# Kernel tuning notes

Hardware: AMD Instinct MI355X
Metric: run time of the kernel (lower is better)

The kernel has to match this reference:

```python
import jax, jax.numpy as jnp
import numpy as np

G = 4096          # number of graphs in the batch
N = 1048576       # total nodes across batch
E = 16777216      # total edges across batch
NUM_RELS = 50     # relation vocabulary


def setup_inputs() -> dict:
    key = jax.random.key(0)
    k0, k1, k2, k3, k4 = jax.random.split(key, 5)
    node_type = jax.random.randint(k0, (N,), 0, 3, dtype=jnp.int32)
    edge_type = jax.random.randint(k1, (E,), 0, NUM_RELS, dtype=jnp.int32)
    edge_index = jax.random.randint(k2, (2, E), 0, N, dtype=jnp.int32)
    edge_batch = jnp.sort(jax.random.randint(k3, (E,), 0, G, dtype=jnp.int32))
    scorer_weight = jax.random.normal(k4, (NUM_RELS * 9, 1), dtype=jnp.float32)
    return {
        "node_type": node_type,
        "edge_type": edge_type,
        "edge_index": edge_index,
        "edge_batch": edge_batch,
        "scorer_weight": scorer_weight,
        "num_graphs": G,
    }


def reference(node_type, edge_type, edge_index, edge_batch, scorer_weight, num_graphs):
    # edge encoding: et*9 + nt[src]*3 + nt[dst]   (per-edge index into table)
    enc = edge_type * 9 + node_type[edge_index[0]] * 3 + node_type[edge_index[1]]
    # embedding lookup (hidden_size == 1) -> [E]
    vals = scorer_weight[enc, 0]
    # per-graph sum of edge scores -> [G]
    per_graph = jax.ops.segment_sum(vals, edge_batch, num_segments=num_graphs)
    # torch.stack([[score], ...]) -> [G, 1]
    return per_graph[:, None]
```

## Files before the change

### kernel.cpp

```cpp
#include <hip/hip_runtime.h>

typedef int v4i __attribute__((ext_vector_type(4)));
typedef unsigned int u32;
typedef __attribute__((address_space(1))) const u32 gas_u32;
typedef __attribute__((address_space(3))) u32 las_u32;

#define THREADS 1024
#define NWAVES (THREADS / 64)
#define EPT 8
#define CHUNK (THREADS * EPT)
#define NBLK 256
#define PART_BITS 19
#define PART_NODES (1 << PART_BITS)
#define PART_WORDS (PART_NODES / 16)
#define TBL 450
#define WAVE_WORDS (PART_WORDS / NWAVES)
#define DMA_PER_WAVE (WAVE_WORDS / 256)

#define BAR() do {                                            \
    asm volatile("s_waitcnt lgkmcnt(0)" ::: "memory");        \
    __builtin_amdgcn_s_barrier();                             \
    __builtin_amdgcn_sched_barrier(0);                        \
} while (0)

#define WAITVM(n) do {                                        \
    asm volatile("s_waitcnt vmcnt(" #n ")" ::: "memory");     \
    __builtin_amdgcn_sched_barrier(0);                        \
} while (0)

__global__ void zero_kernel(float* __restrict__ out, int n) {
    int i = blockIdx.x * blockDim.x + threadIdx.x;
    if (i < n) out[i] = 0.0f;
}

__global__ void pack_nt_kernel(const int* __restrict__ nt,
                               unsigned int* __restrict__ packed,
                               int nwords, int N) {
    int i = blockIdx.x * blockDim.x + threadIdx.x;
    if (i >= nwords) return;
    unsigned int word = 0;
    int base = i * 16;
    if (base + 16 <= N) {
        #pragma unroll
        for (int j = 0; j < 4; ++j) {
            int4 v = *reinterpret_cast<const int4*>(nt + base + j * 4);
            word |= (unsigned)(v.x & 3) << (2 * (j * 4 + 0));
            word |= (unsigned)(v.y & 3) << (2 * (j * 4 + 1));
            word |= (unsigned)(v.z & 3) << (2 * (j * 4 + 2));
            word |= (unsigned)(v.w & 3) << (2 * (j * 4 + 3));
        }
    } else {
        for (int j = 0; base + j < N; ++j)
            word |= (unsigned)(nt[base + j] & 3) << (2 * j);
    }
    packed[i] = word;
}

__device__ __forceinline__ void dma_fill(const u32* __restrict__ pnt,
                                         u32* lds_base, int p, int wv, int lane) {
    const u32* g = pnt + (size_t)p * PART_WORDS + wv * WAVE_WORDS + lane * 4;
    u32* l = lds_base + wv * WAVE_WORDS;
    #pragma unroll
    for (int i = 0; i < DMA_PER_WAVE; ++i)
        __builtin_amdgcn_global_load_lds((gas_u32*)(g + i * 256),
                                         (las_u32*)(l + i * 256), 16, 0, 0);
}

__launch_bounds__(THREADS)
__global__ void edge_score_k(const u32* __restrict__ pnt,
                             const int* __restrict__ et_g,
                             const int* __restrict__ es_g,
                             const int* __restrict__ ed_g,
                             const int* __restrict__ eb_g,
                             const float* __restrict__ wt,
                             float* __restrict__ out,
                             int nchunk) {
    __shared__ __align__(16) u32 buf[PART_WORDS];
    __shared__ float lw[TBL];

    const int tid  = threadIdx.x;
    const int lane = tid & 63;
    const int wv   = tid >> 6;

    if (tid < TBL) lw[tid] = wt[tid];

    const long blk0 = (long)blockIdx.x * ((long)nchunk * CHUNK);
    const long lb   = (long)wv * (64 * EPT) + (long)lane * 4;

    v4i etv[2], svv[2], dvv[2];
    #pragma unroll
    for (int j = 0; j < 2; ++j) {
        etv[j] = __builtin_nontemporal_load((const v4i*)(et_g + blk0 + lb + j * 256));
        svv[j] = __builtin_nontemporal_load((const v4i*)(es_g + blk0 + lb + j * 256));
        dvv[j] = __builtin_nontemporal_load((const v4i*)(ed_g + blk0 + lb + j * 256));
    }

    for (int c = 0; c < nchunk; ++c) {
        const long cb = blk0 + (long)c * CHUNK + lb;

        BAR();
        dma_fill(pnt, buf, 0, wv, lane);
        v4i ebv0 = __builtin_nontemporal_load((const v4i*)(eb_g + cb));
        v4i ebv1 = __builtin_nontemporal_load((const v4i*)(eb_g + cb + 256));
        int sv[EPT], dv[EPT], enc[EPT];
        #pragma unroll
        for (int j = 0; j < 2; ++j)
            #pragma unroll
            for (int q = 0; q < 4; ++q) {
                enc[j * 4 + q] = etv[j][q] * 9;
                sv[j * 4 + q]  = svv[j][q];
                dv[j * 4 + q]  = dvv[j][q];
            }
        WAITVM(2);
        BAR();
        #pragma unroll
        for (int k = 0; k < EPT; ++k) {
            unsigned s = (unsigned)sv[k], d = (unsigned)dv[k];
            bool as = (s >> PART_BITS) == 0u;
            bool ad = (d >> PART_BITS) == 0u;
            u32 ws = buf[as ? ((s >> 4) & (PART_WORDS - 1u)) : 0u];
            u32 wd = buf[ad ? ((d >> 4) & (PART_WORDS - 1u)) : 0u];
            if (as) enc[k] += (int)((ws >> ((s & 15u) << 1)) & 3u) * 3;
            if (ad) enc[k] += (int)((wd >> ((d & 15u) << 1)) & 3u);
        }

        BAR();
        dma_fill(pnt, buf, 1, wv, lane);
        {
            long nb = (c + 1 < nchunk) ? (cb + CHUNK) : cb;
            #pragma unroll
            for (int j = 0; j < 2; ++j) {
                etv[j] = __builtin_nontemporal_load((const v4i*)(et_g + nb + j * 256));
                svv[j] = __builtin_nontemporal_load((const v4i*)(es_g + nb + j * 256));
                dvv[j] = __builtin_nontemporal_load((const v4i*)(ed_g + nb + j * 256));
            }
        }
        WAITVM(6);
        BAR();
        #pragma unroll
        for (int k = 0; k < EPT; ++k) {
            unsigned s = (unsigned)sv[k], d = (unsigned)dv[k];
            bool as = (s >> PART_BITS) == 1u;
            bool ad = (d >> PART_BITS) == 1u;
            u32 ws = buf[as ? ((s >> 4) & (PART_WORDS - 1u)) : 0u];
            u32 wd = buf[ad ? ((d >> 4) & (PART_WORDS - 1u)) : 0u];
            if (as) enc[k] += (int)((ws >> ((s & 15u) << 1)) & 3u) * 3;
            if (ad) enc[k] += (int)((wd >> ((d & 15u) << 1)) & 3u);
        }

        float val[EPT];
        #pragma unroll
        for (int k = 0; k < EPT; ++k) val[k] = lw[enc[k]];

        int wb0 = __shfl(ebv0[0], 0);
        int wbL = __shfl(ebv1[3], 63);
        if (wb0 == wbL) {
            float ssum = 0.0f;
            #pragma unroll
            for (int k = 0; k < EPT; ++k) ssum += val[k];
            #pragma unroll
            for (int off = 32; off >= 1; off >>= 1)
                ssum += __shfl_down(ssum, off);
            if (lane == 0) atomicAdd(&out[wb0], ssum);
        } else {
            float acc = 0.0f; int cur = -1;
            #pragma unroll
            for (int k = 0; k < EPT; ++k) {
                int bb = (k < 4) ? ebv0[k] : ebv1[k - 4];
                if (bb != cur) {
                    if (cur >= 0) atomicAdd(&out[cur], acc);
                    cur = bb; acc = 0.0f;
                }
                acc += val[k];
            }
            if (cur >= 0) atomicAdd(&out[cur], acc);
        }
    }
}

__global__ void edge_score_simple(const int* __restrict__ nt,
                                  const int* __restrict__ et,
                                  const int* __restrict__ es,
                                  const int* __restrict__ ed,
                                  const int* __restrict__ eb,
                                  const float* __restrict__ w,
                                  float* __restrict__ out,
                                  long e0, long E) {
    long e = e0 + (long)blockIdx.x * blockDim.x + threadIdx.x;
    if (e >= E) return;
    int enc = et[e] * 9 + nt[es[e]] * 3 + nt[ed[e]];
    atomicAdd(&out[eb[e]], w[enc]);
}

extern "C" void kernel_launch(void* const* d_in, const int* in_sizes, int n_in,
                              void* d_out, int out_size, void* d_ws, size_t ws_size,
                              hipStream_t stream) {
    const int*   node_type  = (const int*)d_in[0];
    const int*   edge_type  = (const int*)d_in[1];
    const int*   edge_index = (const int*)d_in[2];
    const int*   edge_batch = (const int*)d_in[3];
    const float* w          = (const float*)d_in[4];
    float* out = (float*)d_out;

    long N = in_sizes[0];
    long E = in_sizes[1];
    const int* esrc = edge_index;
    const int* edst = edge_index + E;

    zero_kernel<<<(out_size + 255) / 256, 256, 0, stream>>>(out, out_size);

    int  nwords = (int)((N + 15) / 16);
    long nchunk = E / ((long)NBLK * CHUNK);
    bool fast_ok = (ws_size >= (size_t)nwords * 4) &&
                   (N <= 2L * PART_NODES) && (nchunk > 0);

    if (fast_ok) {
        unsigned int* pnt = (unsigned int*)d_ws;
        pack_nt_kernel<<<(nwords + 255) / 256, 256, 0, stream>>>(node_type, pnt, nwords, (int)N);

        edge_score_k<<<NBLK, THREADS, 0, stream>>>(
            pnt, edge_type, esrc, edst, edge_batch, w, out, (int)nchunk);

        long covered = (long)NBLK * nchunk * CHUNK;
        long rem     = E - covered;
        if (rem > 0) {
            int tb = (int)((rem + 255) / 256);
            edge_score_simple<<<tb, 256, 0, stream>>>(
                node_type, edge_type, esrc, edst, edge_batch, w, out, covered, E);
        }
    } else {
        int tb = (int)((E + 255) / 256);
        edge_score_simple<<<tb, 256, 0, stream>>>(
            node_type, edge_type, esrc, edst, edge_batch, w, out, 0, E);
    }
}
```

Measured before the change: 113.8 us.

## Split node-type table into four LDS partitions with double-buffered DMA fills

Cuts the packed node-type table into four 16K-word partitions and double-buffers them in LDS, so the next partition's DMA fill overlaps the current gather phase instead of refilling a single buffer serially. Per-edge partition byte addresses and shifts are computed once and reused across the four phases, and edges outside the current partition read a zero pad word rather than branching. The edge-data prefetch of the next chunk is dropped in favour of loading at the start of each chunk. The block now goes through four barrier-separated phases per chunk, and each edge does eight LDS reads instead of four, which adds sync and LDS traffic.

After: 152.5 us. 34.1% more time.

```diff
diff --git a/kernel.cpp b/kernel.cpp
--- a/kernel.cpp
+++ b/kernel.cpp
@@ -6,16 +6,18 @@
 typedef __attribute__((address_space(3))) u32 las_u32;
 
 #define THREADS 1024
-#define NWAVES (THREADS / 64)
+#define NWAVES 16
 #define EPT 8
 #define CHUNK (THREADS * EPT)
 #define NBLK 256
-#define PART_BITS 19
+#define PART_BITS 18
 #define PART_NODES (1 << PART_BITS)
 #define PART_WORDS (PART_NODES / 16)
+#define NPART 4
 #define TBL 450
-#define WAVE_WORDS (PART_WORDS / NWAVES)
-#define DMA_PER_WAVE (WAVE_WORDS / 256)
+#define FILL_WAVE_WORDS (PART_WORDS / NWAVES)
+#define FILL_PER_WAVE (FILL_WAVE_WORDS / 256)
+#define ZPAD_BYTE (2u * PART_WORDS * 4u)
 
 #define BAR() do {                                            \
     asm volatile("s_waitcnt lgkmcnt(0)" ::: "memory");        \
@@ -57,13 +59,33 @@
 }
 
 __device__ __forceinline__ void dma_fill(const u32* __restrict__ pnt,
-                                         u32* lds_base, int p, int wv, int lane) {
-    const u32* g = pnt + (size_t)p * PART_WORDS + wv * WAVE_WORDS + lane * 4;
-    u32* l = lds_base + wv * WAVE_WORDS;
+                                         u32* lds0, int p, int wv, int lane) {
+    const u32* g = pnt + (size_t)p * PART_WORDS + wv * FILL_WAVE_WORDS + lane * 4;
+    u32* l = lds0 + (p & 1) * PART_WORDS + wv * FILL_WAVE_WORDS;
     #pragma unroll
-    for (int i = 0; i < DMA_PER_WAVE; ++i)
+    for (int i = 0; i < FILL_PER_WAVE; ++i)
         __builtin_amdgcn_global_load_lds((gas_u32*)(g + i * 256),
                                          (las_u32*)(l + i * 256), 16, 0, 0);
+}
+
+template <int P>
+__device__ __forceinline__ void gather_phase(const u32* lds0,
+                                             const u32 (&axs)[EPT], const u32 (&axd)[EPT],
+                                             const u32 (&shs)[EPT], const u32 (&shd)[EPT],
+                                             int (&enc)[EPT]) {
+    #pragma unroll
+    for (int k = 0; k < EPT; ++k) {
+        u32 as = axs[k];
+        u32 aaddr = ((as & 3u) == (u32)P) ? (as - (u32)P) : ZPAD_BYTE;
+        u32 rs = *reinterpret_cast<const u32*>(
+                     reinterpret_cast<const char*>(lds0) + aaddr);
+        u32 ad = axd[k];
+        u32 daddr = ((ad & 3u) == (u32)P) ? (ad - (u32)P) : ZPAD_BYTE;
+        u32 rd = *reinterpret_cast<const u32*>(
+                     reinterpret_cast<const char*>(lds0) + daddr);
+        enc[k] += (int)((rs >> shs[k]) & 3u) * 3;
+        enc[k] += (int)((rd >> shd[k]) & 3u);
+    }
 }
 
 __launch_bounds__(THREADS)
@@ -75,85 +97,80 @@
                              const float* __restrict__ wt,
                              float* __restrict__ out,
                              int nchunk) {
-    __shared__ __align__(16) u32 buf[PART_WORDS];
-    __shared__ float lw[TBL];
+    __shared__ __align__(16) u32 lds_all[2 * PART_WORDS + 16 + TBL];
+    u32* lds0 = lds_all;
+    float* lw = reinterpret_cast<float*>(lds_all + 2 * PART_WORDS + 16);
 
     const int tid  = threadIdx.x;
     const int lane = tid & 63;
     const int wv   = tid >> 6;
 
-    if (tid < TBL) lw[tid] = wt[tid];
+    if (tid < 16) lds_all[2 * PART_WORDS + tid] = 0u;
+    for (int i = tid; i < TBL; i += THREADS) lw[i] = wt[i];
+
+    dma_fill(pnt, lds0, 0, wv, lane);
 
     const long blk0 = (long)blockIdx.x * ((long)nchunk * CHUNK);
     const long lb   = (long)wv * (64 * EPT) + (long)lane * 4;
 
-    v4i etv[2], svv[2], dvv[2];
-    #pragma unroll
-    for (int j = 0; j < 2; ++j) {
-        etv[j] = __builtin_nontemporal_load((const v4i*)(et_g + blk0 + lb + j * 256));
-        svv[j] = __builtin_nontemporal_load((const v4i*)(es_g + blk0 + lb + j * 256));
-        dvv[j] = __builtin_nontemporal_load((const v4i*)(ed_g + blk0 + lb + j * 256));
-    }
-
     for (int c = 0; c < nchunk; ++c) {
         const long cb = blk0 + (long)c * CHUNK + lb;
 
         BAR();
-        dma_fill(pnt, buf, 0, wv, lane);
-        v4i ebv0 = __builtin_nontemporal_load((const v4i*)(eb_g + cb));
-        v4i ebv1 = __builtin_nontemporal_load((const v4i*)(eb_g + cb + 256));
-        int sv[EPT], dv[EPT], enc[EPT];
+        v4i et0 = __builtin_nontemporal_load((const v4i*)(et_g + cb));
+        v4i et1 = __builtin_nontemporal_load((const v4i*)(et_g + cb + 256));
+        v4i sv0 = __builtin_nontemporal_load((const v4i*)(es_g + cb));
+        v4i sv1 = __builtin_nontemporal_load((const v4i*)(es_g + cb + 256));
+        v4i dv0 = __builtin_nontemporal_load((const v4i*)(ed_g + cb));
+        v4i dv1 = __builtin_nontemporal_load((const v4i*)(ed_g + cb + 256));
+        __builtin_amdgcn_sched_barrier(0);
+        dma_fill(pnt, lds0, 1, wv, lane);
+
+        int enc[EPT]; u32 axs[EPT], axd[EPT], shs[EPT], shd[EPT];
         #pragma unroll
-        for (int j = 0; j < 2; ++j)
-            #pragma unroll
-            for (int q = 0; q < 4; ++q) {
-                enc[j * 4 + q] = etv[j][q] * 9;
-                sv[j * 4 + q]  = svv[j][q];
-                dv[j * 4 + q]  = dvv[j][q];
-            }
-        WAITVM(2);
-        BAR();
-        #pragma unroll
-        for (int k = 0; k < EPT; ++k) {
-            unsigned s = (unsigned)sv[k], d = (unsigned)dv[k];
-            bool as = (s >> PART_BITS) == 0u;
-            bool ad = (d >> PART_BITS) == 0u;
-            u32 ws = buf[as ? ((s >> 4) & (PART_WORDS - 1u)) : 0u];
-            u32 wd = buf[ad ? ((d >> 4) & (PART_WORDS - 1u)) : 0u];
-            if (as) enc[k] += (int)((ws >> ((s & 15u) << 1)) & 3u) * 3;
-            if (ad) enc[k] += (int)((wd >> ((d & 15u) << 1)) & 3u);
-        }
-
-        BAR();
-        dma_fill(pnt, buf, 1, wv, lane);
-        {
-            long nb = (c + 1 < nchunk) ? (cb + CHUNK) : cb;
-            #pragma unroll
-            for (int j = 0; j < 2; ++j) {
-                etv[j] = __builtin_nontemporal_load((const v4i*)(et_g + nb + j * 256));
-                svv[j] = __builtin_nontemporal_load((const v4i*)(es_g + nb + j * 256));
-                dvv[j] = __builtin_nontemporal_load((const v4i*)(ed_g + nb + j * 256));
-            }
-        }
+        for (int q = 0; q < 4; ++q) {
+            enc[q]     = et0[q] * 9;
+            enc[4 + q] = et1[q] * 9;
+            u32 s0 = (u32)sv0[q], s1 = (u32)sv1[q];
+            u32 d0 = (u32)dv0[q], d1 = (u32)dv1[q];
+            axs[q]     = (((s0 >> 4) << 2) & 0x1FFFFu) | (s0 >> PART_BITS);
+            axs[4 + q] = (((s1 >> 4) << 2) & 0x1FFFFu) | (s1 >> PART_BITS);
+            axd[q]     = (((d0 >> 4) << 2) & 0x1FFFFu) | (d0 >> PART_BITS);
+            axd[4 + q] = (((d1 >> 4) << 2) & 0x1FFFFu) | (d1 >> PART_BITS);
+            shs[q]     = (s0 & 15u) << 1;
+            shs[4 + q] = (s1 & 15u) << 1;
+            shd[q]     = (d0 & 15u) << 1;
+            shd[4 + q] = (d1 & 15u) << 1;
+        }
+        BAR();
+        gather_phase<0>(lds0, axs, axd, shs, shd, enc);
+
+        BAR();
+        dma_fill(pnt, lds0, 2, wv, lane);
+        WAITVM(4);
+        BAR();
+        gather_phase<1>(lds0, axs, axd, shs, shd, enc);
+
+        BAR();
+        dma_fill(pnt, lds0, 3, wv, lane);
+        WAITVM(4);
+        BAR();
+        gather_phase<2>(lds0, axs, axd, shs, shd, enc);
+
+        BAR();
+        dma_fill(pnt, lds0, 0, wv, lane);
+        v4i eb0 = __builtin_nontemporal_load((const v4i*)(eb_g + cb));
+        v4i eb1 = __builtin_nontemporal_load((const v4i*)(eb_g + cb + 256));
         WAITVM(6);
         BAR();
-        #pragma unroll
-        for (int k = 0; k < EPT; ++k) {
-            unsigned s = (unsigned)sv[k], d = (unsigned)dv[k];
-            bool as = (s >> PART_BITS) == 1u;
-            bool ad = (d >> PART_BITS) == 1u;
-            u32 ws = buf[as ? ((s >> 4) & (PART_WORDS - 1u)) : 0u];
-            u32 wd = buf[ad ? ((d >> 4) & (PART_WORDS - 1u)) : 0u];
-            if (as) enc[k] += (int)((ws >> ((s & 15u) << 1)) & 3u) * 3;
-            if (ad) enc[k] += (int)((wd >> ((d & 15u) << 1)) & 3u);
-        }
+        gather_phase<3>(lds0, axs, axd, shs, shd, enc);
 
         float val[EPT];
         #pragma unroll
         for (int k = 0; k < EPT; ++k) val[k] = lw[enc[k]];
 
-        int wb0 = __shfl(ebv0[0], 0);
-        int wbL = __shfl(ebv1[3], 63);
+        int wb0 = __shfl(eb0[0], 0);
+        int wbL = __shfl(eb1[3], 63);
         if (wb0 == wbL) {
             float ssum = 0.0f;
             #pragma unroll
@@ -166,7 +183,7 @@
             float acc = 0.0f; int cur = -1;
             #pragma unroll
             for (int k = 0; k < EPT; ++k) {
-                int bb = (k < 4) ? ebv0[k] : ebv1[k - 4];
+                int bb = (k < 4) ? eb0[k] : eb1[k - 4];
                 if (bb != cur) {
                     if (cur >= 0) atomicAdd(&out[cur], acc);
                     cur = bb; acc = 0.0f;
@@ -212,7 +229,7 @@
     int  nwords = (int)((N + 15) / 16);
     long nchunk = E / ((long)NBLK * CHUNK);
     bool fast_ok = (ws_size >= (size_t)nwords * 4) &&
-                   (N <= 2L * PART_NODES) && (nchunk > 0);
+                   (N <= (long)NPART * PART_NODES) && (nchunk > 0);
 
     if (fast_ok) {
         unsigned int* pnt = (unsigned int*)d_ws;
```

## Split edge scoring into two partition passes with 16-bit intermediate encodings

Applied to the files above, without the earlier changes.

Replaces the single kernel that refilled both LDS node-type partitions every chunk with two kernels, each loading one partition into LDS once. The first pass computes the edge-type and partition-0 contributions and stores them as packed 16-bit values. The second pass adds the partition-1 contributions, looks up weights and does the segmented atomic reduction. This removes the repeated LDS refills and barriers per chunk. In exchange it re-reads src/dst indices and adds a write and read of 2 bytes per edge, and it needs a larger workspace or it falls back to the old kernel.

New measurement: 158.7 us. +39.5%, slower.

```diff
diff --git a/kernel.cpp b/kernel.cpp
--- a/kernel.cpp
+++ b/kernel.cpp
@@ -2,11 +2,12 @@
 
 typedef int v4i __attribute__((ext_vector_type(4)));
 typedef unsigned int u32;
+typedef unsigned short u16;
 typedef __attribute__((address_space(1))) const u32 gas_u32;
 typedef __attribute__((address_space(3))) u32 las_u32;
 
 #define THREADS 1024
-#define NWAVES (THREADS / 64)
+#define NWAVES 16
 #define EPT 8
 #define CHUNK (THREADS * EPT)
 #define NBLK 256
@@ -14,15 +15,15 @@
 #define PART_NODES (1 << PART_BITS)
 #define PART_WORDS (PART_NODES / 16)
 #define TBL 450
-#define WAVE_WORDS (PART_WORDS / NWAVES)
-#define DMA_PER_WAVE (WAVE_WORDS / 256)
+#define FILL_WAVE_WORDS (PART_WORDS / NWAVES)
+#define FILL_PER_WAVE (FILL_WAVE_WORDS / 256)
+#define ITER_EDGES ((long)NBLK * THREADS * EPT)
 
 #define BAR() do {                                            \
     asm volatile("s_waitcnt lgkmcnt(0)" ::: "memory");        \
     __builtin_amdgcn_s_barrier();                             \
     __builtin_amdgcn_sched_barrier(0);                        \
 } while (0)
-
 #define WAITVM(n) do {                                        \
     asm volatile("s_waitcnt vmcnt(" #n ")" ::: "memory");     \
     __builtin_amdgcn_sched_barrier(0);                        \
@@ -57,31 +58,147 @@
 }
 
 __device__ __forceinline__ void dma_fill(const u32* __restrict__ pnt,
-                                         u32* lds_base, int p, int wv, int lane) {
-    const u32* g = pnt + (size_t)p * PART_WORDS + wv * WAVE_WORDS + lane * 4;
-    u32* l = lds_base + wv * WAVE_WORDS;
+                                         u32* lds0, int p, int wv, int lane) {
+    const u32* g = pnt + (size_t)p * PART_WORDS + wv * FILL_WAVE_WORDS + lane * 4;
+    u32* l = lds0 + wv * FILL_WAVE_WORDS;
     #pragma unroll
-    for (int i = 0; i < DMA_PER_WAVE; ++i)
+    for (int i = 0; i < FILL_PER_WAVE; ++i)
         __builtin_amdgcn_global_load_lds((gas_u32*)(g + i * 256),
                                          (las_u32*)(l + i * 256), 16, 0, 0);
 }
 
 __launch_bounds__(THREADS)
-__global__ void edge_score_k(const u32* __restrict__ pnt,
-                             const int* __restrict__ et_g,
-                             const int* __restrict__ es_g,
-                             const int* __restrict__ ed_g,
-                             const int* __restrict__ eb_g,
-                             const float* __restrict__ wt,
-                             float* __restrict__ out,
-                             int nchunk) {
-    __shared__ __align__(16) u32 buf[PART_WORDS];
-    __shared__ float lw[TBL];
-
+__global__ void pass_a_kernel(const u32* __restrict__ pnt,
+                              const int* __restrict__ et_g,
+                              const int* __restrict__ es_g,
+                              const int* __restrict__ ed_g,
+                              u16* __restrict__ enc16,
+                              int niter) {
+    __shared__ __align__(16) u32 tbl[PART_WORDS];
     const int tid  = threadIdx.x;
     const int lane = tid & 63;
     const int wv   = tid >> 6;
-
+    dma_fill(pnt, tbl, 0, wv, lane);
+    __syncthreads();
+
+    const long tbase = ((long)blockIdx.x * THREADS + tid) * EPT;
+    for (int it = 0; it < niter; ++it) {
+        const long e0 = tbase + (long)it * ITER_EDGES;
+        v4i et0 = __builtin_nontemporal_load((const v4i*)(et_g + e0));
+        v4i et1 = __builtin_nontemporal_load((const v4i*)(et_g + e0 + 4));
+        v4i sv0 = __builtin_nontemporal_load((const v4i*)(es_g + e0));
+        v4i sv1 = __builtin_nontemporal_load((const v4i*)(es_g + e0 + 4));
+        v4i dv0 = __builtin_nontemporal_load((const v4i*)(ed_g + e0));
+        v4i dv1 = __builtin_nontemporal_load((const v4i*)(ed_g + e0 + 4));
+        u32 w[4];
+        #pragma unroll
+        for (int j = 0; j < 4; ++j) {
+            u32 pairv = 0;
+            #pragma unroll
+            for (int h = 0; h < 2; ++h) {
+                const int k = j * 2 + h;
+                u32 et = (u32)((k < 4) ? et0[k] : et1[k - 4]);
+                u32 s  = (u32)((k < 4) ? sv0[k] : sv1[k - 4]);
+                u32 d  = (u32)((k < 4) ? dv0[k] : dv1[k - 4]);
+                u32 ws = tbl[(s >> 4) & (PART_WORDS - 1u)];
+                u32 wd = tbl[(d >> 4) & (PART_WORDS - 1u)];
+                u32 ts = (ws >> ((s & 15u) << 1)) & 3u;
+                u32 td = (wd >> ((d & 15u) << 1)) & 3u;
+                ts = (s >> PART_BITS) ? 0u : ts;
+                td = (d >> PART_BITS) ? 0u : td;
+                pairv |= (et * 9u + ts * 3u + td) << (h * 16);
+            }
+            w[j] = pairv;
+        }
+        v4i wvec; wvec[0] = (int)w[0]; wvec[1] = (int)w[1];
+        wvec[2] = (int)w[2]; wvec[3] = (int)w[3];
+        *reinterpret_cast<v4i*>(enc16 + e0) = wvec;
+    }
+}
+
+__launch_bounds__(THREADS)
+__global__ void pass_b_kernel(const u32* __restrict__ pnt,
+                              const int* __restrict__ es_g,
+                              const int* __restrict__ ed_g,
+                              const u16* __restrict__ enc16,
+                              const int* __restrict__ eb_g,
+                              const float* __restrict__ wt,
+                              float* __restrict__ out,
+                              int niter) {
+    __shared__ __align__(16) u32 tbl[PART_WORDS + TBL];
+    float* lw = reinterpret_cast<float*>(tbl + PART_WORDS);
+    const int tid  = threadIdx.x;
+    const int lane = tid & 63;
+    const int wv   = tid >> 6;
+    dma_fill(pnt, tbl, 1, wv, lane);
+    for (int i = tid; i < TBL; i += THREADS) lw[i] = wt[i];
+    __syncthreads();
+
+    const long tbase = ((long)blockIdx.x * THREADS + tid) * EPT;
+    for (int it = 0; it < niter; ++it) {
+        const long e0 = tbase + (long)it * ITER_EDGES;
+        v4i sv0 = __builtin_nontemporal_load((const v4i*)(es_g + e0));
+        v4i sv1 = __builtin_nontemporal_load((const v4i*)(es_g + e0 + 4));
+        v4i dv0 = __builtin_nontemporal_load((const v4i*)(ed_g + e0));
+        v4i dv1 = __builtin_nontemporal_load((const v4i*)(ed_g + e0 + 4));
+        v4i ev  = *reinterpret_cast<const v4i*>(enc16 + e0);
+        v4i eb0 = __builtin_nontemporal_load((const v4i*)(eb_g + e0));
+        v4i eb1 = __builtin_nontemporal_load((const v4i*)(eb_g + e0 + 4));
+
+        float val[EPT];
+        #pragma unroll
+        for (int k = 0; k < EPT; ++k) {
+            u32 s = (u32)((k < 4) ? sv0[k] : sv1[k - 4]);
+            u32 d = (u32)((k < 4) ? dv0[k] : dv1[k - 4]);
+            u32 ws = tbl[(s >> 4) & (PART_WORDS - 1u)];
+            u32 wd = tbl[(d >> 4) & (PART_WORDS - 1u)];
+            u32 ts = (ws >> ((s & 15u) << 1)) & 3u;
+            u32 td = (wd >> ((d & 15u) << 1)) & 3u;
+            ts = (s >> PART_BITS) ? ts : 0u;
+            td = (d >> PART_BITS) ? td : 0u;
+            u32 ep = ((u32)ev[k / 2] >> ((k & 1) * 16)) & 0xFFFFu;
+            val[k] = lw[ep + ts * 3u + td];
+        }
+
+        int wb0 = __shfl(eb0[0], 0);
+        int wbL = __shfl(eb1[3], 63);
+        if (wb0 == wbL) {
+            float ssum = ((val[0] + val[1]) + (val[2] + val[3]))
+                       + ((val[4] + val[5]) + (val[6] + val[7]));
+            #pragma unroll
+            for (int off = 32; off >= 1; off >>= 1)
+                ssum += __shfl_down(ssum, off);
+            if (lane == 0) atomicAdd(&out[wb0], ssum);
+        } else {
+            float acc = 0.0f; int cur = -1;
+            #pragma unroll
+            for (int k = 0; k < EPT; ++k) {
+                int bb = (k < 4) ? eb0[k] : eb1[k - 4];
+                if (bb != cur) {
+                    if (cur >= 0) atomicAdd(&out[cur], acc);
+                    cur = bb; acc = 0.0f;
+                }
+                acc += val[k];
+            }
+            if (cur >= 0) atomicAdd(&out[cur], acc);
+        }
+    }
+}
+
+__launch_bounds__(THREADS)
+__global__ void edge_score_r8(const u32* __restrict__ pnt,
+                              const int* __restrict__ et_g,
+                              const int* __restrict__ es_g,
+                              const int* __restrict__ ed_g,
+                              const int* __restrict__ eb_g,
+                              const float* __restrict__ wt,
+                              float* __restrict__ out,
+                              int nchunk) {
+    __shared__ __align__(16) u32 buf[PART_WORDS];
+    __shared__ float lw[TBL];
+    const int tid  = threadIdx.x;
+    const int lane = tid & 63;
+    const int wv   = tid >> 6;
     if (tid < TBL) lw[tid] = wt[tid];
 
     const long blk0 = (long)blockIdx.x * ((long)nchunk * CHUNK);
@@ -97,7 +214,6 @@
 
     for (int c = 0; c < nchunk; ++c) {
         const long cb = blk0 + (long)c * CHUNK + lb;
-
         BAR();
         dma_fill(pnt, buf, 0, wv, lane);
         v4i ebv0 = __builtin_nontemporal_load((const v4i*)(eb_g + cb));
@@ -111,8 +227,7 @@
                 sv[j * 4 + q]  = svv[j][q];
                 dv[j * 4 + q]  = dvv[j][q];
             }
-        WAITVM(2);
-        BAR();
+        WAITVM(2); BAR();
         #pragma unroll
         for (int k = 0; k < EPT; ++k) {
             unsigned s = (unsigned)sv[k], d = (unsigned)dv[k];
@@ -123,7 +238,6 @@
             if (as) enc[k] += (int)((ws >> ((s & 15u) << 1)) & 3u) * 3;
             if (ad) enc[k] += (int)((wd >> ((d & 15u) << 1)) & 3u);
         }
-
         BAR();
         dma_fill(pnt, buf, 1, wv, lane);
         {
@@ -135,8 +249,7 @@
                 dvv[j] = __builtin_nontemporal_load((const v4i*)(ed_g + nb + j * 256));
             }
         }
-        WAITVM(6);
-        BAR();
+        WAITVM(6); BAR();
         #pragma unroll
         for (int k = 0; k < EPT; ++k) {
             unsigned s = (unsigned)sv[k], d = (unsigned)dv[k];
@@ -147,11 +260,9 @@
             if (as) enc[k] += (int)((ws >> ((s & 15u) << 1)) & 3u) * 3;
             if (ad) enc[k] += (int)((wd >> ((d & 15u) << 1)) & 3u);
         }
-
         float val[EPT];
         #pragma unroll
         for (int k = 0; k < EPT; ++k) val[k] = lw[enc[k]];
-
         int wb0 = __shfl(ebv0[0], 0);
         int wbL = __shfl(ebv1[3], 63);
         if (wb0 == wbL) {
@@ -209,18 +320,35 @@
 
     zero_kernel<<<(out_size + 255) / 256, 256, 0, stream>>>(out, out_size);
 
-    int  nwords = (int)((N + 15) / 16);
-    long nchunk = E / ((long)NBLK * CHUNK);
-    bool fast_ok = (ws_size >= (size_t)nwords * 4) &&
-                   (N <= 2L * PART_NODES) && (nchunk > 0);
-
-    if (fast_ok) {
-        unsigned int* pnt = (unsigned int*)d_ws;
+    int    nwords   = (int)((N + 15) / 16);
+    size_t need_pnt = (size_t)2 * PART_WORDS * 4;
+    size_t need_two = need_pnt + (size_t)E * 2;
+    long   niter    = E / ITER_EDGES;
+    long   nchunk   = E / ((long)NBLK * CHUNK);
+    bool   n_ok     = (N <= 2L * PART_NODES);
+
+    if (n_ok && niter > 0 && ws_size >= need_two) {
+        u32* pnt   = (u32*)d_ws;
+        u16* enc16 = (u16*)((char*)d_ws + need_pnt);
         pack_nt_kernel<<<(nwords + 255) / 256, 256, 0, stream>>>(node_type, pnt, nwords, (int)N);
 
-        edge_score_k<<<NBLK, THREADS, 0, stream>>>(
+        pass_a_kernel<<<NBLK, THREADS, 0, stream>>>(
+            pnt, edge_type, esrc, edst, enc16, (int)niter);
+        pass_b_kernel<<<NBLK, THREADS, 0, stream>>>(
+            pnt, esrc, edst, enc16, edge_batch, w, out, (int)niter);
+
+        long covered = niter * ITER_EDGES;
+        long rem     = E - covered;
+        if (rem > 0) {
+            int tb = (int)((rem + 255) / 256);
+            edge_score_simple<<<tb, 256, 0, stream>>>(
+                node_type, edge_type, esrc, edst, edge_batch, w, out, covered, E);
+        }
+    } else if (n_ok && nchunk > 0 && ws_size >= need_pnt) {
+        u32* pnt = (u32*)d_ws;
+        pack_nt_kernel<<<(nwords + 255) / 256, 256, 0, stream>>>(node_type, pnt, nwords, (int)N);
+        edge_score_r8<<<NBLK, THREADS, 0, stream>>>(
             pnt, edge_type, esrc, edst, edge_batch, w, out, (int)nchunk);
-
         long covered = (long)NBLK * nchunk * CHUNK;
         long rem     = E - covered;
         if (rem > 0) {
```
